# Performance work log

Hardware: AMD Instinct MI355X
Metric: run time of the kernel (lower is better)

Reference implementation:

```python
import jax, jax.numpy as jnp
import numpy as np

ITE = 10
R = 3
ALPHA = 1.05

BAND, CHA, HEI, WID = 32, 128, 64, 64


def setup_inputs() -> dict:
    key = jax.random.key(0)
    k1, k2 = jax.random.split(key)
    x = jax.random.normal(k1, (BAND, CHA, HEI, WID), dtype=jnp.float32)
    W = jax.random.uniform(k2, (BAND, CHA, HEI, WID), dtype=jnp.float32)
    x_g = jnp.zeros((BAND, CHA, HEI, WID), dtype=jnp.float32)
    return {"x": x, "W": W, "x_g": x_g}


def reference(x, W, x_g):
    Band, Cha, Hei, Wid = x.shape
    N = Hei * Wid
    xf = x.reshape(Band, Cha, N)
    Wf = W.reshape(Band, Cha, N)
    rho0 = 0.5 * jnp.mean(Wf)

    L0 = xf
    UV0 = jnp.zeros_like(xf)

    def step(carry, _):
        L, rho, _ = carry
        # Gram matrix per band: (Band, Cha, Cha)
        G = jnp.einsum('bcn,bdn->bcd', L, L)
        U, _, _ = jnp.linalg.svd(G, full_matrices=False)
        U = U[:, :, :R]  # top-r left singular vectors
        # UV = U @ (U^T @ L): rank-r projection of L
        UtL = jnp.einsum('bcr,bcn->brn', U, L)
        UV = jnp.einsum('bcr,brn->bcn', U, UtL)
        loss = jnp.mean((UV.reshape(Band, Cha, Hei, Wid) - x_g) ** 2)
        loss_F = jnp.mean(Wf * (UV - xf) ** 2)
        # mu = rho * exp(-log(W + rho)) == rho / (W + rho)
        mu = rho / (Wf + rho)
        L_new = (1.0 - mu) * xf + mu * UV
        return (L_new, rho * ALPHA, UV), (loss_F, loss)

    (_, _, UV), (loss_F, loss) = jax.lax.scan(step, (L0, rho0, UV0), None, length=ITE)
    return UV.reshape(Band, Cha, Hei, Wid), loss_F, loss
```

## Files before the change

kernel.cpp:

```cpp
#include <hip/hip_runtime.h>
#include <stdint.h>

#define BANDS 32
#define CHN   128
#define NPIX  4096
#define NTOT  16777216
#define GSZ   16384
#define KSQ   6

#define L_OFF    1024
#define GP_OFF   (L_OFF + NTOT)
#define A0_OFF   (GP_OFF + BANDS*8*GSZ)
#define A1_OFF   (A0_OFF + BANDS*GSZ)
#define U3_OFF   (A1_OFF + BANDS*GSZ)
#define VW_OFF   (U3_OFF + BANDS*CHN*3)

typedef short s16x8 __attribute__((ext_vector_type(8)));
typedef float f32x4 __attribute__((ext_vector_type(4)));

__device__ __forceinline__ unsigned short bf16rn(float x) {
    uint32_t u = __float_as_uint(x);
    u += 0x7FFFu + ((u >> 16) & 1u);
    return (unsigned short)(u >> 16);
}
__device__ __forceinline__ float bf16tof(unsigned short h) {
    return __uint_as_float((uint32_t)h << 16);
}

__global__ __launch_bounds__(256) void k_init(const float* __restrict__ x,
                                              const float* __restrict__ W,
                                              float* __restrict__ ws) {
    int gid = blockIdx.x * 256 + threadIdx.x;
    const float4* x4 = (const float4*)x;
    const float4* w4 = (const float4*)W;
    float4* L4 = (float4*)(ws + L_OFF);
    float s = 0.f;
#pragma unroll
    for (int i = 0; i < 8; i++) {
        int idx = gid + i * 524288;
        float4 xv = x4[idx];
        float4 wv = w4[idx];
        L4[idx] = xv;
        s += wv.x + wv.y + wv.z + wv.w;
    }
    for (int o = 32; o > 0; o >>= 1) s += __shfl_down(s, o, 64);
    __shared__ float red[4];
    int wid = threadIdx.x >> 6, lane = threadIdx.x & 63;
    if (lane == 0) red[wid] = s;
    __syncthreads();
    if (threadIdx.x == 0) {
        float t = red[0] + red[1] + red[2] + red[3];
        atomicAdd((double*)ws, (double)t);
    }
}

__global__ __launch_bounds__(256) void k_gram(float* __restrict__ ws) {
    int band = blockIdx.y, kc = blockIdx.x, tid = threadIdx.x;
    __shared__ __align__(16) unsigned short Hs[8192];
    __shared__ __align__(16) unsigned short Lo[8192];
    const float* Lb = ws + L_OFF + (size_t)band * CHN * NPIX;
    int k0 = kc * 512;
    int lane = tid & 63, wv = tid >> 6;
    int wr = (wv >> 1) * 64, wcb = (wv & 1) * 64;
    int l15 = lane & 15, l4g = lane >> 4;

    f32x4 acc[4][4];
#pragma unroll
    for (int m = 0; m < 4; m++)
#pragma unroll
        for (int n = 0; n < 4; n++) acc[m][n] = (f32x4){0.f, 0.f, 0.f, 0.f};

    int srow = tid >> 3, scol = (tid & 7) * 8;

    float4 pre[8];
#pragma unroll
    for (int p = 0; p < 4; p++) {
        const float* src = Lb + (size_t)(srow + p * 32) * NPIX + k0 + scol;
        pre[2 * p]     = *(const float4*)src;
        pre[2 * p + 1] = *(const float4*)(src + 4);
    }
#pragma unroll 1
    for (int t = 0; t < 8; t++) {
#pragma unroll
        for (int p = 0; p < 4; p++) {
            int row = srow + p * 32;
            float vv[8] = {pre[2*p].x, pre[2*p].y, pre[2*p].z, pre[2*p].w,
                           pre[2*p+1].x, pre[2*p+1].y, pre[2*p+1].z, pre[2*p+1].w};
            s16x8 hv, lv;
#pragma unroll
            for (int e = 0; e < 8; e++) {
                unsigned short h = bf16rn(vv[e]);
                float r = vv[e] - bf16tof(h);
                hv[e] = (short)h;
                lv[e] = (short)bf16rn(r);
            }
            int off = row * 128 + ((scol * 2) ^ ((row & 7) << 4));
            *(s16x8*)((char*)Hs + off) = hv;
            *(s16x8*)((char*)Lo + off) = lv;
        }
        __syncthreads();
        if (t < 7) {
            int kn = k0 + (t + 1) * 64;
#pragma unroll
            for (int p = 0; p < 4; p++) {
                const float* src = Lb + (size_t)(srow + p * 32) * NPIX + kn + scol;
                pre[2 * p]     = *(const float4*)src;
                pre[2 * p + 1] = *(const float4*)(src + 4);
            }
        }
#pragma unroll
        for (int ks = 0; ks < 2; ks++) {
            int kb2 = ks * 64 + l4g * 16;
            s16x8 Ah[4], Al[4], Bh[4], Bl[4];
#pragma unroll
            for (int m = 0; m < 4; m++) {
                int row = wr + m * 16 + l15;
                int off = row * 128 + (kb2 ^ ((row & 7) << 4));
                Ah[m] = *(const s16x8*)((const char*)Hs + off);
                Al[m] = *(const s16x8*)((const char*)Lo + off);
            }
#pragma unroll
            for (int n = 0; n < 4; n++) {
                int row = wcb + n * 16 + l15;
                int off = row * 128 + (kb2 ^ ((row & 7) << 4));
                Bh[n] = *(const s16x8*)((const char*)Hs + off);
                Bl[n] = *(const s16x8*)((const char*)Lo + off);
            }
#pragma unroll
            for (int m = 0; m < 4; m++)
#pragma unroll
                for (int n = 0; n < 4; n++) {
                    acc[m][n] = __builtin_amdgcn_mfma_f32_16x16x32_bf16(Ah[m], Bh[n], acc[m][n], 0, 0, 0);
                    acc[m][n] = __builtin_amdgcn_mfma_f32_16x16x32_bf16(Ah[m], Bl[n], acc[m][n], 0, 0, 0);
                    acc[m][n] = __builtin_amdgcn_mfma_f32_16x16x32_bf16(Al[m], Bh[n], acc[m][n], 0, 0, 0);
                }
        }
        __syncthreads();
    }
    float* Gp = ws + GP_OFF + (size_t)(band * 8 + kc) * GSZ;
#pragma unroll
    for (int m = 0; m < 4; m++)
#pragma unroll
        for (int n = 0; n < 4; n++) {
            int row0 = wr + m * 16 + l4g * 4;
            int col  = wcb + n * 16 + l15;
#pragma unroll
            for (int r = 0; r < 4; r++)
                Gp[(row0 + r) * 128 + col] = acc[m][n][r];
        }
}

__global__ __launch_bounds__(256) void k_eig(float* __restrict__ ws, int titer) {
    int band = blockIdx.x, tid = threadIdx.x;
    __shared__ __align__(16) float Aa[128 * 132];
    __shared__ __align__(16) unsigned short HiS[128 * 128];
    __shared__ __align__(16) unsigned short LoS[128 * 128];
    __shared__ __align__(16) float VcS[8 * 136];
    __shared__ __align__(16) float WcS[8 * 136];
    __shared__ float LchS[64], invdS[8], B8S[64], E8S[64], redS[8];
    __shared__ int idx3S[3];

    int lane = tid & 63, wv = tid >> 6;
    int l15 = lane & 15, l4g = lane >> 4;
    int wr = (wv >> 1) * 64, wcb = (wv & 1) * 64;

    const float4* Gp4 = (const float4*)(ws + GP_OFF + (size_t)band * 8 * GSZ);
    float fp = 0.f, tp = 0.f;
#pragma unroll
    for (int rep = 0; rep < 16; rep++) {
        int fi4 = rep * 256 + tid;
        float4 v = Gp4[fi4];
#pragma unroll
        for (int p = 1; p < 8; p++) {
            float4 u = Gp4[p * 4096 + fi4];
            v.x += u.x; v.y += u.y; v.z += u.z; v.w += u.w;
        }
        int r = fi4 >> 5, c4 = (fi4 & 31) * 4;
        *(float4*)&Aa[r * 132 + c4] = v;
        fp += v.x*v.x + v.y*v.y + v.z*v.z + v.w*v.w;
        int e = r - c4;
        if (e >= 0 && e < 4) tp += (&v.x)[e];
    }
#pragma unroll
    for (int o = 1; o < 64; o <<= 1) { fp += __shfl_xor(fp, o, 64); tp += __shfl_xor(tp, o, 64); }
    if (lane == 0) { redS[wv] = fp; redS[4 + wv] = tp; }
    __syncthreads();
    fp = (redS[0] + redS[1]) + (redS[2] + redS[3]);
    tp = (redS[4] + redS[5]) + (redS[6] + redS[7]);

    for (int j = 0; j < KSQ; j++) {
        if (tp * tp < 3.5f * fp) break;
        float s2 = 1.0f / fp;
#pragma unroll
        for (int rep = 0; rep < 8; rep++) {
            int idx8 = rep * 256 + tid;
            int row = idx8 >> 4, c8 = (idx8 & 15) * 8;
            float4 v0 = *(const float4*)&Aa[row * 132 + c8];
            float4 v1 = *(const float4*)&Aa[row * 132 + c8 + 4];
            float vv[8] = {v0.x, v0.y, v0.z, v0.w, v1.x, v1.y, v1.z, v1.w};
            s16x8 hv, lv;
#pragma unroll
            for (int e = 0; e < 8; e++) {
                unsigned short h = bf16rn(vv[e]);
                float r = vv[e] - bf16tof(h);
                hv[e] = (short)h;
                lv[e] = (short)bf16rn(r);
            }
            int off = row * 256 + ((c8 * 2) ^ ((row & 7) << 4));
            *(s16x8*)((char*)HiS + off) = hv;
            *(s16x8*)((char*)LoS + off) = lv;
        }
        __syncthreads();
        f32x4 acc[4][4];
#pragma unroll
        for (int m = 0; m < 4; m++)
#pragma unroll
            for (int n = 0; n < 4; n++) acc[m][n] = (f32x4){0.f, 0.f, 0.f, 0.f};
#pragma unroll
        for (int ks = 0; ks < 4; ks++) {
            int kb = ks * 64 + l4g * 16;
            s16x8 Ah[4], Al[4], Bh[4], Bl[4];
#pragma unroll
            for (int m = 0; m < 4; m++) {
                int row = wr + m * 16 + l15;
                int off = row * 256 + (kb ^ ((row & 7) << 4));
                Ah[m] = *(const s16x8*)((const char*)HiS + off);
                Al[m] = *(const s16x8*)((const char*)LoS + off);
            }
#pragma unroll
            for (int n = 0; n < 4; n++) {
                int row = wcb + n * 16 + l15;
                int off = row * 256 + (kb ^ ((row & 7) << 4));
                Bh[n] = *(const s16x8*)((const char*)HiS + off);
                Bl[n] = *(const s16x8*)((const char*)LoS + off);
            }
#pragma unroll
            for (int m = 0; m < 4; m++)
#pragma unroll
                for (int n = 0; n < 4; n++) {
                    acc[m][n] = __builtin_amdgcn_mfma_f32_16x16x32_bf16(Ah[m], Bh[n], acc[m][n], 0, 0, 0);
                    acc[m][n] = __builtin_amdgcn_mfma_f32_16x16x32_bf16(Ah[m], Bl[n], acc[m][n], 0, 0, 0);
                    acc[m][n] = __builtin_amdgcn_mfma_f32_16x16x32_bf16(Al[m], Bh[n], acc[m][n], 0, 0, 0);
                }
        }
        float nfp = 0.f, ntp = 0.f;
#pragma unroll
        for (int m = 0; m < 4; m++)
#pragma unroll
            for (int n = 0; n < 4; n++)
#pragma unroll
                for (int r = 0; r < 4; r++) {
                    int row = wr + m * 16 + l4g * 4 + r;
                    int col = wcb + n * 16 + l15;
                    float val = s2 * acc[m][n][r];
                    Aa[row * 132 + col] = val;
                    nfp += val * val;
                    if (row == col) ntp += val;
                }
#pragma unroll
        for (int o = 1; o < 64; o <<= 1) { nfp += __shfl_xor(nfp, o, 64); ntp += __shfl_xor(ntp, o, 64); }
        if (lane == 0) { redS[wv] = nfp; redS[4 + wv] = ntp; }
        __syncthreads();
        fp = (redS[0] + redS[1]) + (redS[2] + redS[3]);
        tp = (redS[4] + redS[5]) + (redS[6] + redS[7]);
    }

    if (titer == 0) {
        for (int idx = tid; idx < 1024; idx += 256) {
            uint32_t h = (uint32_t)(idx + band * 1024 + 7) * 2654435761u;
            h ^= h >> 15; h *= 0x2c1b3c6du; h ^= h >> 12;
            VcS[(idx >> 7) * 136 + (idx & 127)] = ((float)(h & 0xFFFF) / 32768.0f) - 1.0f;
        }
    } else {
        for (int idx = tid; idx < 1024; idx += 256)
            VcS[(idx >> 7) * 136 + (idx & 127)] = ws[VW_OFF + band * 1024 + idx];
    }
    __syncthreads();

    int c = tid & 127, sq = tid >> 7;
    int r8 = tid >> 3, s8 = tid & 7;
    int steps = (titer == 0) ? 8 : 4;

    for (int step = 0; step <= steps; step++) {
        {
            const float* V0 = VcS + (sq * 4 + 0) * 136;
            const float* V1 = VcS + (sq * 4 + 1) * 136;
            const float* V2 = VcS + (sq * 4 + 2) * 136;
            const float* V3 = VcS + (sq * 4 + 3) * 136;
            float a0 = 0.f, a1 = 0.f, a2 = 0.f, a3 = 0.f;
#pragma unroll 4
            for (int k = 0; k < 128; k += 4) {
                float g0 = Aa[(k + 0) * 132 + c];
                float g1 = Aa[(k + 1) * 132 + c];
                float g2 = Aa[(k + 2) * 132 + c];
                float g3 = Aa[(k + 3) * 132 + c];
                float4 v0 = *(const float4*)&V0[k];
                float4 v1 = *(const float4*)&V1[k];
                float4 v2 = *(const float4*)&V2[k];
                float4 v3 = *(const float4*)&V3[k];
                a0 += g0 * v0.x + g1 * v0.y + g2 * v0.z + g3 * v0.w;
                a1 += g0 * v1.x + g1 * v1.y + g2 * v1.z + g3 * v1.w;
                a2 += g0 * v2.x + g1 * v2.y + g2 * v2.z + g3 * v2.w;
                a3 += g0 * v3.x + g1 * v3.y + g2 * v3.z + g3 * v3.w;
            }
            WcS[(sq * 4 + 0) * 136 + c] = a0;
            WcS[(sq * 4 + 1) * 136 + c] = a1;
            WcS[(sq * 4 + 2) * 136 + c] = a2;
            WcS[(sq * 4 + 3) * 136 + c] = a3;
        }
        __syncthreads();
        if (step == steps) break;

        if (tid < 64) {
            const float* wrp = WcS + r8 * 136;
            const float* wcp = WcS + s8 * 136;
            float m = 0.f;
#pragma unroll 8
            for (int k = 0; k < 128; k += 4) {
                float4 p = *(const float4*)&wrp[k];
                float4 q = *(const float4*)&wcp[k];
                m += p.x * q.x + p.y * q.y + p.z * q.z + p.w * q.w;
            }
            float t = (r8 == s8) ? m : 0.f;
#pragma unroll
            for (int o = 1; o < 64; o <<= 1) t += __shfl_xor(t, o, 64);
            float eps = 1e-12f * t + 1e-35f;
            float v = m;
#pragma unroll
            for (int j = 0; j < 8; j++) {
                float dj = __shfl(v, j * 9, 64);
                dj = fmaxf(dj, eps);
                float lj = sqrtf(dj);
                float inv = 1.f / lj;
                if (s8 == j) v = (r8 == j) ? lj : (r8 > j ? v * inv : v);
                float Lr = __shfl(v, r8 * 8 + j, 64);
                float Ls = __shfl(v, s8 * 8 + j, 64);
                if (r8 > j && s8 > j) v -= Lr * Ls;
                if (tid == j) invdS[j] = inv;
            }
            LchS[tid] = v;
        }
        __syncthreads();
        if (tid < 128) {
            float w[8], vv[8];
#pragma unroll
            for (int s = 0; s < 8; s++) w[s] = WcS[s * 136 + tid];
#pragma unroll
            for (int s = 0; s < 8; s++) {
                float t2 = w[s];
                for (int j = 0; j < s; j++) t2 -= vv[j] * LchS[s * 8 + j];
                vv[s] = t2 * invdS[s];
                VcS[s * 136 + tid] = vv[s];
            }
        }
        __syncthreads();
    }

    if (tid < 64) {
        const float* vr = VcS + r8 * 136;
        const float* wcp = WcS + s8 * 136;
        float m = 0.f;
#pragma unroll 8
        for (int k = 0; k < 128; k += 4) {
            float4 p = *(const float4*)&vr[k];
            float4 q = *(const float4*)&wcp[k];
            m += p.x * q.x + p.y * q.y + p.z * q.z + p.w * q.w;
        }
        float mT = __shfl(m, s8 * 8 + r8, 64);
        float b = 0.5f * (m + mT);
        float e = (r8 == s8) ? 1.f : 0.f;

        for (int sweep = 0; sweep < 6; sweep++) {
            for (int rd = 0; rd < 7; rd++) {
                int pr = (r8 == 7) ? rd : ((r8 == rd) ? 7 : (2 * rd + 7 - r8) % 7);
                int pc = (s8 == 7) ? rd : ((s8 == rd) ? 7 : (2 * rd + 7 - s8) % 7);
                int P = min(r8, pr), Q = max(r8, pr);
                int Pc = min(s8, pc), Qc = max(s8, pc);
                float app = __shfl(b, P * 9, 64);
                float aqq = __shfl(b, Q * 9, 64);
                float apq = __shfl(b, P * 8 + Q, 64);
                float cR, sR;
                if (fabsf(apq) < 1e-28f) { cR = 1.f; sR = 0.f; }
                else {
                    float tau = (aqq - app) / (2.f * apq);
                    float tt = ((tau >= 0.f) ? 1.f : -1.f) / (fabsf(tau) + sqrtf(1.f + tau * tau));
                    cR = rsqrtf(1.f + tt * tt); sR = tt * cR;
                }
                float ap2 = __shfl(b, Pc * 9, 64);
                float aq2 = __shfl(b, Qc * 9, 64);
                float apq2 = __shfl(b, Pc * 8 + Qc, 64);
                float cC, sC;
                if (fabsf(apq2) < 1e-28f) { cC = 1.f; sC = 0.f; }
                else {
                    float tau = (aq2 - ap2) / (2.f * apq2);
                    float tt = ((tau >= 0.f) ? 1.f : -1.f) / (fabsf(tau) + sqrtf(1.f + tau * tau));
                    cC = rsqrtf(1.f + tt * tt); sC = tt * cC;
                }
                float tv = __shfl(b, pr * 8 + s8, 64);
                float bn = (r8 < pr) ? (cR * b - sR * tv) : (sR * tv + cR * b);
                float t2 = __shfl(bn, r8 * 8 + pc, 64);
                b = (s8 < pc) ? (cC * bn - sC * t2) : (sC * t2 + cC * bn);
                float e2 = __shfl(e, r8 * 8 + pc, 64);
                e = (s8 < pc) ? (cC * e - sC * e2) : (sC * e2 + cC * e);
            }
        }
        B8S[tid] = b;
        E8S[tid] = e;
        if (tid == 0) {
            int used = 0;
            for (int r = 0; r < 3; r++) {
                int best = 0; float bv = -1e38f;
                for (int s = 0; s < 8; s++)
                    if (!(used & (1 << s)) && B8S[s * 9] > bv) { bv = B8S[s * 9]; best = s; }
                used |= 1 << best;
                idx3S[r] = best;
            }
        }
    }
    __syncthreads();

    if (tid < 128) {
        float e[3][8];
#pragma unroll
        for (int r = 0; r < 3; r++)
#pragma unroll
            for (int s = 0; s < 8; s++) e[r][s] = E8S[s * 8 + idx3S[r]];
        float vcl[8];
#pragma unroll
        for (int s = 0; s < 8; s++) vcl[s] = VcS[s * 136 + tid];
#pragma unroll
        for (int r = 0; r < 3; r++) {
            float u = 0.f;
#pragma unroll
            for (int s = 0; s < 8; s++) u += vcl[s] * e[r][s];
            ws[U3_OFF + band * 384 + tid * 3 + r] = u;
        }
#pragma unroll
        for (int s = 0; s < 8; s++) ws[VW_OFF + band * 1024 + s * 128 + tid] = vcl[s];
    }
}

__global__ __launch_bounds__(256) void k_upd(const float* __restrict__ x,
                                             const float* __restrict__ W,
                                             const float* __restrict__ xg,
                                             float* __restrict__ out,
                                             float* __restrict__ ws,
                                             float alphapow, int writeUV, int titer) {
    int band = blockIdx.y, xc = blockIdx.x, tid = threadIdx.x;
    int w = tid >> 6, lane = tid & 63;
    int half = lane >> 5, l32 = lane & 31;
    int n0 = xc * 128, p4 = l32 * 4;
    int cs = w * 2 + half;
    __shared__ float Us[128][4];
    __shared__ __align__(16) float up[24][132];
    __shared__ __align__(16) float um[3][132];
    __shared__ float red[16];

    if (tid < 128) {
        Us[tid][0] = ws[U3_OFF + band * 384 + tid * 3 + 0];
        Us[tid][1] = ws[U3_OFF + band * 384 + tid * 3 + 1];
        Us[tid][2] = ws[U3_OFF + band * 384 + tid * 3 + 2];
    }
    __syncthreads();

    const float* Lb = ws + L_OFF + (size_t)band * CHN * NPIX;
    float4 a0 = make_float4(0.f,0.f,0.f,0.f), a1 = a0, a2 = a0;
#pragma unroll 4
    for (int cg = 0; cg < 16; cg++) {
        int c = cg * 8 + cs;
        float4 lv = *(const float4*)(Lb + (size_t)c * NPIX + n0 + p4);
        float u0 = Us[c][0], u1 = Us[c][1], u2 = Us[c][2];
        a0.x += u0 * lv.x; a0.y += u0 * lv.y; a0.z += u0 * lv.z; a0.w += u0 * lv.w;
        a1.x += u1 * lv.x; a1.y += u1 * lv.y; a1.z += u1 * lv.z; a1.w += u1 * lv.w;
        a2.x += u2 * lv.x; a2.y += u2 * lv.y; a2.z += u2 * lv.z; a2.w += u2 * lv.w;
    }
    *(float4*)&up[cs * 3 + 0][p4] = a0;
    *(float4*)&up[cs * 3 + 1][p4] = a1;
    *(float4*)&up[cs * 3 + 2][p4] = a2;
    __syncthreads();
    if (tid < 96) {
        int r = tid >> 5, p = (tid & 31) * 4;
        float4 s = make_float4(0.f,0.f,0.f,0.f);
#pragma unroll
        for (int g = 0; g < 8; g++) {
            float4 u = *(float4*)&up[g * 3 + r][p];
            s.x += u.x; s.y += u.y; s.z += u.z; s.w += u.w;
        }
        *(float4*)&um[r][p] = s;
    }
    __syncthreads();

    double sw = *(const double*)ws;
    float rho = 0.5f * (float)(sw / (double)NTOT) * alphapow;
    float4 t0 = *(float4*)&um[0][p4];
    float4 t1 = *(float4*)&um[1][p4];
    float4 t2 = *(float4*)&um[2][p4];
    float lf = 0.f, ll = 0.f;
    size_t base = (size_t)band * CHN * NPIX + n0 + p4;
    float* Lp = ws + L_OFF;
#pragma unroll 4
    for (int cg = 0; cg < 16; cg++) {
        int c = cg * 8 + cs;
        size_t idx = base + (size_t)c * NPIX;
        float4 xv = *(const float4*)(x + idx);
        float4 wv = *(const float4*)(W + idx);
        float4 gv = *(const float4*)(xg + idx);
        float u0 = Us[c][0], u1 = Us[c][1], u2 = Us[c][2];
        float4 uv, ln;
        uv.x = u0 * t0.x + u1 * t1.x + u2 * t2.x;
        uv.y = u0 * t0.y + u1 * t1.y + u2 * t2.y;
        uv.z = u0 * t0.z + u1 * t1.z + u2 * t2.z;
        uv.w = u0 * t0.w + u1 * t1.w + u2 * t2.w;
        float dx0 = uv.x - xv.x, dx1 = uv.y - xv.y, dx2 = uv.z - xv.z, dx3 = uv.w - xv.w;
        lf += wv.x * dx0 * dx0 + wv.y * dx1 * dx1 + wv.z * dx2 * dx2 + wv.w * dx3 * dx3;
        float g0 = uv.x - gv.x, g1 = uv.y - gv.y, g2 = uv.z - gv.z, g3 = uv.w - gv.w;
        ll += g0 * g0 + g1 * g1 + g2 * g2 + g3 * g3;
        ln.x = xv.x + (rho / (wv.x + rho)) * dx0;
        ln.y = xv.y + (rho / (wv.y + rho)) * dx1;
        ln.z = xv.z + (rho / (wv.z + rho)) * dx2;
        ln.w = xv.w + (rho / (wv.w + rho)) * dx3;
        *(float4*)(Lp + idx) = ln;
        if (writeUV) *(float4*)(out + idx) = uv;
    }
    for (int o = 32; o > 0; o >>= 1) { lf += __shfl_down(lf, o, 64); ll += __shfl_down(ll, o, 64); }
    if (lane == 0) { red[w] = lf; red[8 + w] = ll; }
    __syncthreads();
    if (tid == 0) {
        float a = red[0] + red[1] + red[2] + red[3];
        float b = red[8] + red[9] + red[10] + red[11];
        atomicAdd((double*)ws + 1 + titer,  (double)a);
        atomicAdd((double*)ws + 11 + titer, (double)b);
    }
}

__global__ void k_final(float* __restrict__ out, const float* __restrict__ ws) {
    int tid = threadIdx.x;
    const double* d = (const double*)ws;
    if (tid < 10)       out[NTOT + tid] = (float)(d[1 + tid] / (double)NTOT);
    else if (tid < 20)  out[NTOT + tid] = (float)(d[11 + (tid - 10)] / (double)NTOT);
}

extern "C" void kernel_launch(void* const* d_in, const int* in_sizes, int n_in,
                              void* d_out, int out_size, void* d_ws, size_t ws_size,
                              hipStream_t stream) {
    const float* x  = (const float*)d_in[0];
    const float* W  = (const float*)d_in[1];
    const float* xg = (const float*)d_in[2];
    float* out = (float*)d_out;
    float* ws = (float*)d_ws;

    hipMemsetAsync(d_ws, 0, 4096, stream);
    k_init<<<2048, 256, 0, stream>>>(x, W, ws);

    float ap = 1.0f;
    for (int t = 0; t < 10; t++) {
        k_gram<<<dim3(8, 32), 256, 0, stream>>>(ws);
        k_eig<<<32, 256, 0, stream>>>(ws, t);
        k_upd<<<dim3(32, 32), 256, 0, stream>>>(x, W, xg, out, ws, ap, (t == 9) ? 1 : 0, t);
        ap *= 1.05f;
    }
    k_final<<<1, 64, 0, stream>>>(out, ws);
}
```

Measured before the change: 1.902 ms.

## Widen eig kernel to 1024 threads and use MFMA for subspace iteration matvec

Raises the per-band eigen kernel from 256 to 1024 threads, retiling the Gram-squaring MFMA so each of the 16 waves computes a 32x32 tile. The G*V product inside subspace iteration moves from scalar FMA loops to split-bf16 MFMA (hi/lo) on a pre-converted copy of the matrix. The 8x8 W^T W Gram is split across four waves with a shared-memory partial reduction. The goal is to shorten this latency-bound single-block-per-band kernel, at the cost of more barriers and bf16x3 precision in the matvec.

```diff
diff --git a/kernel.cpp b/kernel.cpp
--- a/kernel.cpp
+++ b/kernel.cpp
@@ -150,25 +150,30 @@
         }
 }
 
-__global__ __launch_bounds__(256) void k_eig(float* __restrict__ ws, int titer) {
+__global__ __launch_bounds__(1024, 4) void k_eig(float* __restrict__ ws, int titer) {
     int band = blockIdx.x, tid = threadIdx.x;
     __shared__ __align__(16) float Aa[128 * 132];
-    __shared__ __align__(16) unsigned short HiS[128 * 128];
-    __shared__ __align__(16) unsigned short LoS[128 * 128];
+    __shared__ __align__(16) unsigned short HiS[16384];
+    __shared__ __align__(16) unsigned short LoS[16384];
+    __shared__ __align__(16) unsigned short VhB[2048];
+    __shared__ __align__(16) unsigned short VlB[2048];
     __shared__ __align__(16) float VcS[8 * 136];
     __shared__ __align__(16) float WcS[8 * 136];
-    __shared__ float LchS[64], invdS[8], B8S[64], E8S[64], redS[8];
+    __shared__ float LchS[64], invdS[8], B8S[64], E8S[64], redS[32], Mpart[256];
     __shared__ int idx3S[3];
+    float* WpS = Aa;
 
     int lane = tid & 63, wv = tid >> 6;
     int l15 = lane & 15, l4g = lane >> 4;
-    int wr = (wv >> 1) * 64, wcb = (wv & 1) * 64;
+
+    { int off = (8 + (tid >> 7)) * 128 + (tid & 127);
+      VhB[off] = 0; VlB[off] = 0; }
 
     const float4* Gp4 = (const float4*)(ws + GP_OFF + (size_t)band * 8 * GSZ);
     float fp = 0.f, tp = 0.f;
 #pragma unroll
-    for (int rep = 0; rep < 16; rep++) {
-        int fi4 = rep * 256 + tid;
+    for (int rep = 0; rep < 4; rep++) {
+        int fi4 = rep * 1024 + tid;
         float4 v = Gp4[fi4];
 #pragma unroll
         for (int p = 1; p < 8; p++) {
@@ -183,17 +188,18 @@
     }
 #pragma unroll
     for (int o = 1; o < 64; o <<= 1) { fp += __shfl_xor(fp, o, 64); tp += __shfl_xor(tp, o, 64); }
-    if (lane == 0) { redS[wv] = fp; redS[4 + wv] = tp; }
-    __syncthreads();
-    fp = (redS[0] + redS[1]) + (redS[2] + redS[3]);
-    tp = (redS[4] + redS[5]) + (redS[6] + redS[7]);
-
+    if (lane == 0) { redS[wv] = fp; redS[16 + wv] = tp; }
+    __syncthreads();
+    fp = 0.f; tp = 0.f;
+    for (int i = 0; i < 16; i++) { fp += redS[i]; tp += redS[16 + i]; }
+
+    int tr = (wv >> 2) * 32, tc = (wv & 3) * 32;
     for (int j = 0; j < KSQ; j++) {
         if (tp * tp < 3.5f * fp) break;
         float s2 = 1.0f / fp;
 #pragma unroll
-        for (int rep = 0; rep < 8; rep++) {
-            int idx8 = rep * 256 + tid;
+        for (int rep = 0; rep < 2; rep++) {
+            int idx8 = rep * 1024 + tid;
             int row = idx8 >> 4, c8 = (idx8 & 15) * 8;
             float4 v0 = *(const float4*)&Aa[row * 132 + c8];
             float4 v1 = *(const float4*)&Aa[row * 132 + c8 + 4];
@@ -211,33 +217,33 @@
             *(s16x8*)((char*)LoS + off) = lv;
         }
         __syncthreads();
-        f32x4 acc[4][4];
-#pragma unroll
-        for (int m = 0; m < 4; m++)
-#pragma unroll
-            for (int n = 0; n < 4; n++) acc[m][n] = (f32x4){0.f, 0.f, 0.f, 0.f};
+        f32x4 acc[2][2];
+#pragma unroll
+        for (int m = 0; m < 2; m++)
+#pragma unroll
+            for (int n = 0; n < 2; n++) acc[m][n] = (f32x4){0.f, 0.f, 0.f, 0.f};
 #pragma unroll
         for (int ks = 0; ks < 4; ks++) {
             int kb = ks * 64 + l4g * 16;
-            s16x8 Ah[4], Al[4], Bh[4], Bl[4];
-#pragma unroll
-            for (int m = 0; m < 4; m++) {
-                int row = wr + m * 16 + l15;
+            s16x8 Ah[2], Al[2], Bh[2], Bl[2];
+#pragma unroll
+            for (int m = 0; m < 2; m++) {
+                int row = tr + m * 16 + l15;
                 int off = row * 256 + (kb ^ ((row & 7) << 4));
                 Ah[m] = *(const s16x8*)((const char*)HiS + off);
                 Al[m] = *(const s16x8*)((const char*)LoS + off);
             }
 #pragma unroll
-            for (int n = 0; n < 4; n++) {
-                int row = wcb + n * 16 + l15;
+            for (int n = 0; n < 2; n++) {
+                int row = tc + n * 16 + l15;
                 int off = row * 256 + (kb ^ ((row & 7) << 4));
                 Bh[n] = *(const s16x8*)((const char*)HiS + off);
                 Bl[n] = *(const s16x8*)((const char*)LoS + off);
             }
 #pragma unroll
-            for (int m = 0; m < 4; m++)
-#pragma unroll
-                for (int n = 0; n < 4; n++) {
+            for (int m = 0; m < 2; m++)
+#pragma unroll
+                for (int n = 0; n < 2; n++) {
                     acc[m][n] = __builtin_amdgcn_mfma_f32_16x16x32_bf16(Ah[m], Bh[n], acc[m][n], 0, 0, 0);
                     acc[m][n] = __builtin_amdgcn_mfma_f32_16x16x32_bf16(Ah[m], Bl[n], acc[m][n], 0, 0, 0);
                     acc[m][n] = __builtin_amdgcn_mfma_f32_16x16x32_bf16(Al[m], Bh[n], acc[m][n], 0, 0, 0);
@@ -245,13 +251,13 @@
         }
         float nfp = 0.f, ntp = 0.f;
 #pragma unroll
-        for (int m = 0; m < 4; m++)
-#pragma unroll
-            for (int n = 0; n < 4; n++)
+        for (int m = 0; m < 2; m++)
+#pragma unroll
+            for (int n = 0; n < 2; n++)
 #pragma unroll
                 for (int r = 0; r < 4; r++) {
-                    int row = wr + m * 16 + l4g * 4 + r;
-                    int col = wcb + n * 16 + l15;
+                    int row = tr + m * 16 + l4g * 4 + r;
+                    int col = tc + n * 16 + l15;
                     float val = s2 * acc[m][n][r];
                     Aa[row * 132 + col] = val;
                     nfp += val * val;
@@ -259,68 +265,103 @@
                 }
 #pragma unroll
         for (int o = 1; o < 64; o <<= 1) { nfp += __shfl_xor(nfp, o, 64); ntp += __shfl_xor(ntp, o, 64); }
-        if (lane == 0) { redS[wv] = nfp; redS[4 + wv] = ntp; }
-        __syncthreads();
-        fp = (redS[0] + redS[1]) + (redS[2] + redS[3]);
-        tp = (redS[4] + redS[5]) + (redS[6] + redS[7]);
-    }
+        if (lane == 0) { redS[wv] = nfp; redS[16 + wv] = ntp; }
+        __syncthreads();
+        fp = 0.f; tp = 0.f;
+        for (int i = 0; i < 16; i++) { fp += redS[i]; tp += redS[16 + i]; }
+    }
+
+#pragma unroll
+    for (int rep = 0; rep < 2; rep++) {
+        int idx8 = rep * 1024 + tid;
+        int row = idx8 >> 4, c8 = (idx8 & 15) * 8;
+        float4 v0 = *(const float4*)&Aa[row * 132 + c8];
+        float4 v1 = *(const float4*)&Aa[row * 132 + c8 + 4];
+        float vv[8] = {v0.x, v0.y, v0.z, v0.w, v1.x, v1.y, v1.z, v1.w};
+        s16x8 hv, lv;
+#pragma unroll
+        for (int e = 0; e < 8; e++) {
+            unsigned short h = bf16rn(vv[e]);
+            float r = vv[e] - bf16tof(h);
+            hv[e] = (short)h;
+            lv[e] = (short)bf16rn(r);
+        }
+        int off = row * 256 + ((c8 * 2) ^ ((row & 7) << 4));
+        *(s16x8*)((char*)HiS + off) = hv;
+        *(s16x8*)((char*)LoS + off) = lv;
+    }
+    __syncthreads();
 
     if (titer == 0) {
-        for (int idx = tid; idx < 1024; idx += 256) {
+        for (int idx = tid; idx < 1024; idx += 1024) {
             uint32_t h = (uint32_t)(idx + band * 1024 + 7) * 2654435761u;
             h ^= h >> 15; h *= 0x2c1b3c6du; h ^= h >> 12;
             VcS[(idx >> 7) * 136 + (idx & 127)] = ((float)(h & 0xFFFF) / 32768.0f) - 1.0f;
         }
     } else {
-        for (int idx = tid; idx < 1024; idx += 256)
+        for (int idx = tid; idx < 1024; idx += 1024)
             VcS[(idx >> 7) * 136 + (idx & 127)] = ws[VW_OFF + band * 1024 + idx];
     }
     __syncthreads();
 
-    int c = tid & 127, sq = tid >> 7;
-    int r8 = tid >> 3, s8 = tid & 7;
     int steps = (titer == 0) ? 8 : 4;
+    int mt = wv >> 1, kh = wv & 1;
+    int rr = (tid & 63) >> 3, ss = tid & 7;
 
     for (int step = 0; step <= steps; step++) {
+        if (tid < 512) {
+            int jj = tid >> 6, k0 = (tid & 63) * 2;
+            float v0 = VcS[jj * 136 + k0], v1 = VcS[jj * 136 + k0 + 1];
+            unsigned short h0 = bf16rn(v0); float r0 = v0 - bf16tof(h0);
+            unsigned short h1 = bf16rn(v1); float r1 = v1 - bf16tof(h1);
+            int boff = jj * 256 + ((k0 * 2) ^ ((jj & 7) << 4));
+            *(ushort2*)((char*)VhB + boff) = make_ushort2(h0, h1);
+            *(ushort2*)((char*)VlB + boff) = make_ushort2(bf16rn(r0), bf16rn(r1));
+        }
+        __syncthreads();
+        f32x4 acc = (f32x4){0.f, 0.f, 0.f, 0.f};
+#pragma unroll
+        for (int kq = 0; kq < 2; kq++) {
+            int kb = (kh * 2 + kq) * 64 + l4g * 16;
+            int ar = mt * 16 + l15;
+            int aoff = ar * 256 + (kb ^ ((ar & 7) << 4));
+            s16x8 Ah = *(const s16x8*)((const char*)HiS + aoff);
+            s16x8 Al = *(const s16x8*)((const char*)LoS + aoff);
+            int boff = l15 * 256 + (kb ^ ((l15 & 7) << 4));
+            s16x8 Bh = *(const s16x8*)((const char*)VhB + boff);
+            s16x8 Bl = *(const s16x8*)((const char*)VlB + boff);
+            acc = __builtin_amdgcn_mfma_f32_16x16x32_bf16(Ah, Bh, acc, 0, 0, 0);
+            acc = __builtin_amdgcn_mfma_f32_16x16x32_bf16(Ah, Bl, acc, 0, 0, 0);
+            acc = __builtin_amdgcn_mfma_f32_16x16x32_bf16(Al, Bh, acc, 0, 0, 0);
+        }
+        *(f32x4*)&WpS[wv * 256 + lane * 4] = acc;
+        __syncthreads();
         {
-            const float* V0 = VcS + (sq * 4 + 0) * 136;
-            const float* V1 = VcS + (sq * 4 + 1) * 136;
-            const float* V2 = VcS + (sq * 4 + 2) * 136;
-            const float* V3 = VcS + (sq * 4 + 3) * 136;
-            float a0 = 0.f, a1 = 0.f, a2 = 0.f, a3 = 0.f;
-#pragma unroll 4
-            for (int k = 0; k < 128; k += 4) {
-                float g0 = Aa[(k + 0) * 132 + c];
-                float g1 = Aa[(k + 1) * 132 + c];
-                float g2 = Aa[(k + 2) * 132 + c];
-                float g3 = Aa[(k + 3) * 132 + c];
-                float4 v0 = *(const float4*)&V0[k];
-                float4 v1 = *(const float4*)&V1[k];
-                float4 v2 = *(const float4*)&V2[k];
-                float4 v3 = *(const float4*)&V3[k];
-                a0 += g0 * v0.x + g1 * v0.y + g2 * v0.z + g3 * v0.w;
-                a1 += g0 * v1.x + g1 * v1.y + g2 * v1.z + g3 * v1.w;
-                a2 += g0 * v2.x + g1 * v2.y + g2 * v2.z + g3 * v2.w;
-                a3 += g0 * v3.x + g1 * v3.y + g2 * v3.z + g3 * v3.w;
-            }
-            WcS[(sq * 4 + 0) * 136 + c] = a0;
-            WcS[(sq * 4 + 1) * 136 + c] = a1;
-            WcS[(sq * 4 + 2) * 136 + c] = a2;
-            WcS[(sq * 4 + 3) * 136 + c] = a3;
+            int mt2 = tid >> 7, rem = tid & 127;
+            int col = rem & 7, r = (rem >> 3) & 3, g4 = rem >> 5;
+            int lidx = (g4 * 16 + col) * 4 + r;
+            float wval = WpS[(2 * mt2) * 256 + lidx] + WpS[(2 * mt2 + 1) * 256 + lidx];
+            WcS[col * 136 + mt2 * 16 + g4 * 4 + r] = wval;
         }
         __syncthreads();
         if (step == steps) break;
 
-        if (tid < 64) {
-            const float* wrp = WcS + r8 * 136;
-            const float* wcp = WcS + s8 * 136;
+        if (tid < 256) {
+            const float* wrp = WcS + rr * 136 + wv * 32;
+            const float* wcp = WcS + ss * 136 + wv * 32;
             float m = 0.f;
-#pragma unroll 8
-            for (int k = 0; k < 128; k += 4) {
+#pragma unroll
+            for (int k = 0; k < 32; k += 4) {
                 float4 p = *(const float4*)&wrp[k];
                 float4 q = *(const float4*)&wcp[k];
                 m += p.x * q.x + p.y * q.y + p.z * q.z + p.w * q.w;
             }
+            Mpart[wv * 64 + (tid & 63)] = m;
+        }
+        __syncthreads();
+        if (tid < 64) {
+            float m = (Mpart[tid] + Mpart[64 + tid]) + (Mpart[128 + tid] + Mpart[192 + tid]);
+            int r8 = tid >> 3, s8 = tid & 7;
             float t = (r8 == s8) ? m : 0.f;
 #pragma unroll
             for (int o = 1; o < 64; o <<= 1) t += __shfl_xor(t, o, 64);
@@ -356,16 +397,22 @@
         __syncthreads();
     }
 
-    if (tid < 64) {
-        const float* vr = VcS + r8 * 136;
-        const float* wcp = WcS + s8 * 136;
+    if (tid < 256) {
+        const float* vr = VcS + rr * 136 + wv * 32;
+        const float* wcp = WcS + ss * 136 + wv * 32;
         float m = 0.f;
-#pragma unroll 8
-        for (int k = 0; k < 128; k += 4) {
+#pragma unroll
+        for (int k = 0; k < 32; k += 4) {
             float4 p = *(const float4*)&vr[k];
             float4 q = *(const float4*)&wcp[k];
             m += p.x * q.x + p.y * q.y + p.z * q.z + p.w * q.w;
         }
+        Mpart[wv * 64 + (tid & 63)] = m;
+    }
+    __syncthreads();
+    if (tid < 64) {
+        int r8 = tid >> 3, s8 = tid & 7;
+        float m = (Mpart[tid] + Mpart[64 + tid]) + (Mpart[128 + tid] + Mpart[192 + tid]);
         float mT = __shfl(m, s8 * 8 + r8, 64);
         float b = 0.5f * (m + mT);
         float e = (r8 == s8) ? 1.f : 0.f;
@@ -555,7 +602,7 @@
     float ap = 1.0f;
     for (int t = 0; t < 10; t++) {
         k_gram<<<dim3(8, 32), 256, 0, stream>>>(ws);
-        k_eig<<<32, 256, 0, stream>>>(ws, t);
+        k_eig<<<32, 1024, 0, stream>>>(ws, t);
         k_upd<<<dim3(32, 32), 256, 0, stream>>>(x, W, xg, out, ws, ap, (t == 9) ? 1 : 0, t);
         ap *= 1.05f;
     }
```

Measured after the change: 1.658 ms. 12.8% less time.
